# Kernel optimization log

Hardware: AMD Instinct MI355X
Metric: run time of the kernel (lower is better)

The kernel has to match this reference:

```python
import jax, jax.numpy as jnp
import numpy as np

# Standard SMPL kinematic tree (parent of joint i); root parent is -1.
PARENTS = [-1, 0, 0, 0, 1, 2, 3, 4, 5, 6, 7, 8, 9, 9, 9, 12, 13, 14, 16, 17, 18, 19, 20, 21]
NUM_JOINTS = 24
NUM_VERTICES = 6890
NUM_BETAS = 10
UNIT_FACTOR = 1.0  # unit='m'


def rotvec2mat(r):
    """Rodrigues formula. r: (..., 3) -> (..., 3, 3)."""
    theta = jnp.linalg.norm(r, axis=-1, keepdims=True)            # (..., 1)
    safe_theta = jnp.where(theta < 1e-8, 1.0, theta)
    axis = r / safe_theta
    x, y, z = axis[..., 0], axis[..., 1], axis[..., 2]
    zeros = jnp.zeros_like(x)
    K = jnp.stack([zeros, -z, y, z, zeros, -x, -y, x, zeros], axis=-1)
    K = K.reshape(r.shape[:-1] + (3, 3))
    t = theta[..., None]                                          # (..., 1, 1)
    eye = jnp.eye(3, dtype=r.dtype)
    return eye + jnp.sin(t) * K + (1.0 - jnp.cos(t)) * (K @ K)


def setup_inputs() -> dict:
    key = jax.random.key(0)
    ks = jax.random.split(key, 9)
    B = 1024
    pose_rotvecs = 0.3 * jax.random.normal(ks[0], (B, NUM_JOINTS, 3), jnp.float32)
    shape_betas = jax.random.normal(ks[1], (B, NUM_BETAS), jnp.float32)
    trans = jax.random.normal(ks[2], (B, 3), jnp.float32)
    v_template = jax.random.normal(ks[3], (NUM_VERTICES, 3), jnp.float32)
    shapedirs = 0.01 * jax.random.normal(ks[4], (NUM_VERTICES, 3, NUM_BETAS), jnp.float32)
    posedirs = 0.01 * jax.random.normal(ks[5], (NUM_VERTICES, 3, (NUM_JOINTS - 1) * 9), jnp.float32)
    J_template = jax.random.normal(ks[6], (NUM_JOINTS, 3), jnp.float32)
    J_shapedirs = 0.01 * jax.random.normal(ks[7], (NUM_JOINTS, 3, NUM_BETAS), jnp.float32)
    w = jax.random.uniform(ks[8], (NUM_VERTICES, NUM_JOINTS), jnp.float32)
    weights = w / jnp.sum(w, axis=-1, keepdims=True)  # skinning weights: rows sum to 1
    return dict(pose_rotvecs=pose_rotvecs, shape_betas=shape_betas, trans=trans,
                v_template=v_template, shapedirs=shapedirs, posedirs=posedirs,
                J_template=J_template, J_shapedirs=J_shapedirs, weights=weights)


def reference(pose_rotvecs, shape_betas, trans, v_template, shapedirs, posedirs,
              J_template, J_shapedirs, weights):
    B = pose_rotvecs.shape[0]
    parent_idx = jnp.asarray(PARENTS[1:], dtype=jnp.int32)  # (J-1,)

    # Parent-relative rotation matrices from rotation vectors.
    rel_rotmats = rotvec2mat(pose_rotvecs)                  # (B, J, 3, 3)

    # Kinematic chain: compose global rotations along the tree (J=24, fixed small loop).
    glob_list = [rel_rotmats[:, 0]]
    for i in range(1, NUM_JOINTS):
        glob_list.append(glob_list[PARENTS[i]] @ rel_rotmats[:, i])
    glob_rotmats = jnp.stack(glob_list, axis=1)             # (B, J, 3, 3)

    eye = jnp.broadcast_to(jnp.eye(3, dtype=rel_rotmats.dtype), (B, 1, 3, 3))
    parent_glob = jnp.concatenate([eye, glob_rotmats[:, parent_idx]], axis=1)  # (B, J, 3, 3)

    # Shaped joint locations (kid_factor = 0 default -> term vanishes).
    j = J_template + jnp.einsum('jcs,bs->bjc', J_shapedirs, shape_betas)       # (B, J, 3)
    j_parent = jnp.concatenate([jnp.zeros((B, 1, 3), j.dtype), j[:, parent_idx]], axis=1)
    bones = j - j_parent
    rotated_bones = jnp.einsum('bjCc,bjc->bjC', parent_glob, bones)

    pos_list = [j[:, 0]]
    for i in range(1, NUM_JOINTS):
        pos_list.append(pos_list[PARENTS[i]] + rotated_bones[:, i])
    glob_positions = jnp.stack(pos_list, axis=1)            # (B, J, 3)

    # Blendshapes: shape + pose correctives (kid term zero).
    pose_feature = rel_rotmats[:, 1:].reshape(B, (NUM_JOINTS - 1) * 9)
    v_posed = (v_template
               + jnp.einsum('vcp,bp->bvc', shapedirs, shape_betas)
               + jnp.einsum('vcp,bp->bvc', posedirs, pose_feature))            # (B, V, 3)

    # Linear blend skinning.
    translations = glob_positions - jnp.einsum('bjCc,bjc->bjC', glob_rotmats, j)  # (B, J, 3)
    blended_rot = jnp.einsum('vj,bjCc->bvCc', weights, glob_rotmats)              # (B, V, 3, 3)
    vertices = (jnp.einsum('bvCc,bvc->bvC', blended_rot, v_posed)
                + jnp.einsum('vj,bjc->bvc', weights, translations))               # (B, V, 3)

    joints = (glob_positions + trans[:, None]) * UNIT_FACTOR
    vertices = (vertices + trans[:, None]) * UNIT_FACTOR
    return joints, vertices, glob_rotmats
```

## Files before the change

### kernel.cpp

```cpp
#include <hip/hip_runtime.h>
#include <math.h>

#define NJ 24
#define NV 6890
#define NB 10
#define KREAL 217
#define KP 224
#define NVT 432

typedef __attribute__((ext_vector_type(8))) short bf16x8;
typedef __attribute__((ext_vector_type(8))) unsigned short u16x8;
typedef __attribute__((ext_vector_type(4))) float f32x4;

__device__ __forceinline__ unsigned short f2bf(float x) {
    unsigned int u = __float_as_uint(x);
    u += 0x7fffu + ((u >> 16) & 1u);
    return (unsigned short)(u >> 16);
}

__device__ __constant__ int c_path[NJ][9] = {
  {0,0,0,0,0,0,0,0,0},
  {0,1,0,0,0,0,0,0,0},
  {0,2,0,0,0,0,0,0,0},
  {0,3,0,0,0,0,0,0,0},
  {0,1,4,0,0,0,0,0,0},
  {0,2,5,0,0,0,0,0,0},
  {0,3,6,0,0,0,0,0,0},
  {0,1,4,7,0,0,0,0,0},
  {0,2,5,8,0,0,0,0,0},
  {0,3,6,9,0,0,0,0,0},
  {0,1,4,7,10,0,0,0,0},
  {0,2,5,8,11,0,0,0,0},
  {0,3,6,9,12,0,0,0,0},
  {0,3,6,9,13,0,0,0,0},
  {0,3,6,9,14,0,0,0,0},
  {0,3,6,9,12,15,0,0,0},
  {0,3,6,9,13,16,0,0,0},
  {0,3,6,9,14,17,0,0,0},
  {0,3,6,9,13,16,18,0,0},
  {0,3,6,9,14,17,19,0,0},
  {0,3,6,9,13,16,18,20,0},
  {0,3,6,9,14,17,19,21,0},
  {0,3,6,9,13,16,18,20,22},
  {0,3,6,9,14,17,19,21,23}};
__device__ __constant__ int c_plen[NJ] = {1,2,2,2,3,3,3,4,4,4,5,5,5,5,5,6,6,6,7,7,8,8,9,9};

__global__ __launch_bounds__(256)
void pack_kernel(const float* __restrict__ shapedirs, const float* __restrict__ posedirs,
                 unsigned short* __restrict__ dirsF)
{
    __shared__ unsigned short tile[16][3][240];
    const int t = threadIdx.x;
    const int vtg = blockIdx.x;

    for (int idx = t; idx < 16 * 3 * KP; idx += 256) {
        const int v_l = idx / (3 * KP);
        const int rem = idx - v_l * (3 * KP);
        const int c = rem / KP;
        const int k = rem - c * KP;
        const int v = vtg * 16 + v_l;
        float val = 0.f;
        if (v < NV && k < KREAL)
            val = (k < NB) ? shapedirs[(size_t)v * 30 + c * NB + k]
                           : posedirs[(size_t)v * 621 + c * 207 + (k - NB)];
        tile[v_l][c][k] = f2bf(val);
    }
    __syncthreads();

    const int lane = t & 63;
    const int w = t >> 6;
    const int kg = lane >> 4;
    const int vsub = lane & 15;
    for (int j2 = w; j2 < 21; j2 += 4) {
        const int kt = j2 / 3;
        const int c = j2 - kt * 3;
        const u16x8 o = *(const u16x8*)&tile[vsub][c][kt * 32 + kg * 8];
        *(u16x8*)&dirsF[(((size_t)(kt * 3 + c) * NVT + vtg) * 64 + lane) * 8] = o;
    }
}

__global__ __launch_bounds__(64)
void prep_kernel(const float* __restrict__ pose, const float* __restrict__ betas,
                 const float* __restrict__ trans, const float* __restrict__ J_template,
                 const float* __restrict__ J_shapedirs,
                 float* __restrict__ joints_out, float* __restrict__ glob_out,
                 float* __restrict__ A_ws, unsigned short* __restrict__ coeffF, int B)
{
    const int b = blockIdx.x;
    const int t = threadIdx.x;
    __shared__ float s_beta[NB];
    __shared__ float s_rel[NJ][9];
    __shared__ float s_glob[NJ][9];
    __shared__ float s_j[NJ][3];

    if (t < NB) s_beta[t] = betas[b * NB + t];
    __syncthreads();

    if (t < NJ) {
        float rx = pose[b * 72 + t * 3 + 0];
        float ry = pose[b * 72 + t * 3 + 1];
        float rz = pose[b * 72 + t * 3 + 2];
        float th = sqrtf(rx * rx + ry * ry + rz * rz);
        float safe = (th < 1e-8f) ? 1.0f : th;
        float ax = rx / safe, ay = ry / safe, az = rz / safe;
        float s = sinf(th), c = cosf(th), omc = 1.0f - c;
        float aa = ax * ax + ay * ay + az * az;
        float K[9] = {0.f, -az, ay, az, 0.f, -ax, -ay, ax, 0.f};
        float A2[9] = {ax*ax - aa, ax*ay,      ax*az,
                       ay*ax,      ay*ay - aa, ay*az,
                       az*ax,      az*ay,      az*az - aa};
        #pragma unroll
        for (int r = 0; r < 3; ++r)
            #pragma unroll
            for (int cc = 0; cc < 3; ++cc)
                s_rel[t][r * 3 + cc] = ((r == cc) ? 1.0f : 0.0f)
                                     + s * K[r * 3 + cc] + omc * A2[r * 3 + cc];
        #pragma unroll
        for (int cc = 0; cc < 3; ++cc) {
            float acc = J_template[t * 3 + cc];
            #pragma unroll
            for (int q = 0; q < NB; ++q)
                acc = fmaf(J_shapedirs[(t * 3 + cc) * NB + q], s_beta[q], acc);
            s_j[t][cc] = acc;
        }
    }
    __syncthreads();

    if (t < NJ) {
        const int L = c_plen[t];
        float G[9];
        #pragma unroll
        for (int e = 0; e < 9; ++e) G[e] = s_rel[0][e];
        for (int sIdx = 1; sIdx < L; ++sIdx) {
            const int p = c_path[t][sIdx];
            float Tn[9];
            #pragma unroll
            for (int r = 0; r < 3; ++r)
                #pragma unroll
                for (int cc = 0; cc < 3; ++cc)
                    Tn[r * 3 + cc] = G[r * 3 + 0] * s_rel[p][0 * 3 + cc]
                                   + G[r * 3 + 1] * s_rel[p][1 * 3 + cc]
                                   + G[r * 3 + 2] * s_rel[p][2 * 3 + cc];
            #pragma unroll
            for (int e = 0; e < 9; ++e) G[e] = Tn[e];
        }
        #pragma unroll
        for (int e = 0; e < 9; ++e) s_glob[t][e] = G[e];
        #pragma unroll
        for (int e = 0; e < 9; ++e) glob_out[(size_t)b * 216 + t * 9 + e] = G[e];
    }
    __syncthreads();

    if (t < NJ) {
        const int L = c_plen[t];
        float px = s_j[0][0], py = s_j[0][1], pz = s_j[0][2];
        for (int sIdx = 1; sIdx < L; ++sIdx) {
            const int pk = c_path[t][sIdx];
            const int pp = c_path[t][sIdx - 1];
            float bx = s_j[pk][0] - s_j[pp][0];
            float by = s_j[pk][1] - s_j[pp][1];
            float bz = s_j[pk][2] - s_j[pp][2];
            px += s_glob[pp][0] * bx + s_glob[pp][1] * by + s_glob[pp][2] * bz;
            py += s_glob[pp][3] * bx + s_glob[pp][4] * by + s_glob[pp][5] * bz;
            pz += s_glob[pp][6] * bx + s_glob[pp][7] * by + s_glob[pp][8] * bz;
        }
        const float tx = trans[b * 3 + 0], ty = trans[b * 3 + 1], tz = trans[b * 3 + 2];
        joints_out[(size_t)b * 72 + t * 3 + 0] = px + tx;
        joints_out[(size_t)b * 72 + t * 3 + 1] = py + ty;
        joints_out[(size_t)b * 72 + t * 3 + 2] = pz + tz;
        const float jx = s_j[t][0], jy = s_j[t][1], jz = s_j[t][2];
        float T0 = px - (s_glob[t][0] * jx + s_glob[t][1] * jy + s_glob[t][2] * jz) + tx;
        float T1 = py - (s_glob[t][3] * jx + s_glob[t][4] * jy + s_glob[t][5] * jz) + ty;
        float T2 = pz - (s_glob[t][6] * jx + s_glob[t][7] * jy + s_glob[t][8] * jz) + tz;
        float* Ab = A_ws + ((size_t)b * NJ + t) * 12;
        Ab[0]  = s_glob[t][0]; Ab[1]  = s_glob[t][1]; Ab[2]  = s_glob[t][2]; Ab[3]  = T0;
        Ab[4]  = s_glob[t][3]; Ab[5]  = s_glob[t][4]; Ab[6]  = s_glob[t][5]; Ab[7]  = T1;
        Ab[8]  = s_glob[t][6]; Ab[9]  = s_glob[t][7]; Ab[10] = s_glob[t][8]; Ab[11] = T2;
    }
    __syncthreads();

    const int btg = b >> 4, bl = b & 15;
    for (int k = t; k < KP; k += 64) {
        float val;
        if (k < NB) val = s_beta[k];
        else if (k < KREAL) { const int p2 = k - NB; val = s_rel[1 + p2 / 9][p2 % 9]; }
        else val = 0.f;
        const int kt = k >> 5, kg = (k >> 3) & 3, i = k & 7;
        coeffF[(((size_t)kt * (B >> 4) + btg) * 64 + kg * 16 + bl) * 8 + i] = f2bf(val);
    }
}

__global__ __launch_bounds__(256, 4)
void vert_kernel(const float4* __restrict__ dirsF, const float4* __restrict__ coeffF,
                 const float* __restrict__ A_ws, const float* __restrict__ v_template,
                 const float* __restrict__ weights, float* __restrict__ vert_out, int B)
{
    __shared__ float smem[6336];
    const int tid  = threadIdx.x;
    const int lane = tid & 63;
    const int w    = __builtin_amdgcn_readfirstlane(tid >> 6);
    const int vt   = w;
    const int vb4  = blockIdx.y * 4;
    const int bblk = blockIdx.x;
    const int nbt  = B >> 4;

    f32x4 acc[3][4];
    #pragma unroll
    for (int c = 0; c < 3; ++c)
        #pragma unroll
        for (int bt = 0; bt < 4; ++bt) {
            acc[c][bt][0] = 0.f; acc[c][bt][1] = 0.f; acc[c][bt][2] = 0.f; acc[c][bt][3] = 0.f;
        }

    for (int kt = 0; kt < 7; ++kt) {
        __syncthreads();
        #pragma unroll
        for (int s = 0; s < 3; ++s) {
            const int row = s * 256 + tid;
            const int ch = row >> 6, l2 = row & 63;
            *(float4*)&smem[row * 4] =
                dirsF[((size_t)(kt * 3 + (ch >> 2)) * NVT + vb4 + (ch & 3)) * 64 + l2];
        }
        __syncthreads();
        bf16x8 bq[4];
        #pragma unroll
        for (int bt = 0; bt < 4; ++bt)
            bq[bt] = *(const bf16x8*)&coeffF[((size_t)kt * nbt + bblk * 4 + bt) * 64 + lane];
        #pragma unroll
        for (int c = 0; c < 3; ++c) {
            const bf16x8 a = *(const bf16x8*)&smem[((c * 4 + vt) * 64 + lane) * 4];
            #pragma unroll
            for (int bt = 0; bt < 4; ++bt)
                acc[c][bt] = __builtin_amdgcn_mfma_f32_16x16x32_bf16(a, bq[bt], acc[c][bt], 0, 0, 0);
        }
    }

    const int vrow0 = (vb4 + vt) * 16 + ((lane >> 4) << 2);
    #pragma unroll
    for (int c = 0; c < 3; ++c) {
        float tv[4];
        #pragma unroll
        for (int r = 0; r < 4; ++r) {
            const int v = vrow0 + r;
            tv[r] = (v < NV) ? v_template[(size_t)v * 3 + c] : 0.f;
        }
        #pragma unroll
        for (int bt = 0; bt < 4; ++bt) {
            acc[c][bt][0] += tv[0]; acc[c][bt][1] += tv[1];
            acc[c][bt][2] += tv[2]; acc[c][bt][3] += tv[3];
        }
    }

    const int vglob = vb4 * 16 + lane;
    float wj[NJ];
    if (vglob < NV) {
        const float4* wp = (const float4*)(weights + (size_t)vglob * NJ);
        #pragma unroll
        for (int q = 0; q < 6; ++q) {
            const float4 t4 = wp[q];
            wj[q * 4 + 0] = t4.x; wj[q * 4 + 1] = t4.y; wj[q * 4 + 2] = t4.z; wj[q * 4 + 3] = t4.w;
        }
    }

    __syncthreads();

    for (int p = 0; p < 2; ++p) {
        if (p) __syncthreads();
        #pragma unroll
        for (int c = 0; c < 3; ++c)
            #pragma unroll
            for (int half = 0; half < 2; ++half) {
                const int b32 = half * 16 + (lane & 15);
                const int vl  = vt * 16 + ((lane >> 4) << 2);
                const f32x4 av = acc[c][2 * p + half];
                #pragma unroll
                for (int r = 0; r < 4; ++r)
                    smem[(c * 32 + b32) * 66 + vl + r] = av[r];
            }
        __syncthreads();

        if (vglob < NV) {
            for (int i = 0; i < 8; ++i) {
                const int b32 = w * 8 + i;
                const int b = bblk * 64 + p * 32 + b32;
                const float4* Ab = (const float4*)(A_ws + (size_t)b * (NJ * 12));
                float R0 = 0.f, R1 = 0.f, R2 = 0.f, R3 = 0.f, R4 = 0.f, R5 = 0.f,
                      R6 = 0.f, R7 = 0.f, R8 = 0.f, T0 = 0.f, T1 = 0.f, T2 = 0.f;
                #pragma unroll
                for (int jj = 0; jj < NJ; ++jj) {
                    const float wv = wj[jj];
                    const float4 a0 = Ab[jj * 3 + 0];
                    const float4 a1 = Ab[jj * 3 + 1];
                    const float4 a2 = Ab[jj * 3 + 2];
                    R0 = fmaf(wv, a0.x, R0); R1 = fmaf(wv, a0.y, R1); R2 = fmaf(wv, a0.z, R2); T0 = fmaf(wv, a0.w, T0);
                    R3 = fmaf(wv, a1.x, R3); R4 = fmaf(wv, a1.y, R4); R5 = fmaf(wv, a1.z, R5); T1 = fmaf(wv, a1.w, T1);
                    R6 = fmaf(wv, a2.x, R6); R7 = fmaf(wv, a2.y, R7); R8 = fmaf(wv, a2.z, R8); T2 = fmaf(wv, a2.w, T2);
                }
                const float vp0 = smem[(0 * 32 + b32) * 66 + lane];
                const float vp1 = smem[(1 * 32 + b32) * 66 + lane];
                const float vp2 = smem[(2 * 32 + b32) * 66 + lane];
                const float o0 = R0 * vp0 + R1 * vp1 + R2 * vp2 + T0;
                const float o1 = R3 * vp0 + R4 * vp1 + R5 * vp2 + T1;
                const float o2 = R6 * vp0 + R7 * vp1 + R8 * vp2 + T2;
                const size_t off = (size_t)b * (NV * 3) + (size_t)vglob * 3;
                vert_out[off + 0] = o0;
                vert_out[off + 1] = o1;
                vert_out[off + 2] = o2;
            }
        }
    }
}

extern "C" void kernel_launch(void* const* d_in, const int* in_sizes, int n_in,
                              void* d_out, int out_size, void* d_ws, size_t ws_size,
                              hipStream_t stream) {
    const float* pose        = (const float*)d_in[0];
    const float* betas       = (const float*)d_in[1];
    const float* trans       = (const float*)d_in[2];
    const float* v_template  = (const float*)d_in[3];
    const float* shapedirs   = (const float*)d_in[4];
    const float* posedirs    = (const float*)d_in[5];
    const float* J_template  = (const float*)d_in[6];
    const float* J_shapedirs = (const float*)d_in[7];
    const float* weights     = (const float*)d_in[8];
    const int B = in_sizes[0] / 72;

    float* out = (float*)d_out;
    float* joints_out = out;
    float* vert_out   = out + (size_t)B * 72;
    float* glob_out   = out + (size_t)B * 72 + (size_t)B * NV * 3;

    char* ws = (char*)d_ws;
    const size_t a_bytes     = (size_t)B * 288 * 4;
    const size_t coeff_bytes = (size_t)7 * (B >> 4) * 64 * 16;
    float*          A_ws   = (float*)ws;
    unsigned short* coeffF = (unsigned short*)(ws + a_bytes);
    unsigned short* dirsF  = (unsigned short*)(ws + a_bytes + coeff_bytes);

    pack_kernel<<<dim3(NVT), 256, 0, stream>>>(shapedirs, posedirs, dirsF);
    prep_kernel<<<dim3(B), 64, 0, stream>>>(pose, betas, trans, J_template, J_shapedirs,
                                            joints_out, glob_out, A_ws, coeffF, B);
    vert_kernel<<<dim3(B / 64, 108), 256, 0, stream>>>((const float4*)dirsF, (const float4*)coeffF,
                                                       A_ws, v_template, weights, vert_out, B);
}
```

Before: 221.4 us.

## Compute skinning blend with split-bf16 MFMA instead of scalar FMAs

```diff
diff --git a/kernel.cpp b/kernel.cpp
--- a/kernel.cpp
+++ b/kernel.cpp
@@ -16,6 +16,9 @@
     unsigned int u = __float_as_uint(x);
     u += 0x7fffu + ((u >> 16) & 1u);
     return (unsigned short)(u >> 16);
+}
+__device__ __forceinline__ float bf2f(unsigned short h) {
+    return __uint_as_float(((unsigned int)h) << 16);
 }
 
 __device__ __constant__ int c_path[NJ][9] = {
@@ -84,7 +87,8 @@
                  const float* __restrict__ trans, const float* __restrict__ J_template,
                  const float* __restrict__ J_shapedirs,
                  float* __restrict__ joints_out, float* __restrict__ glob_out,
-                 float* __restrict__ A_ws, unsigned short* __restrict__ coeffF, int B)
+                 unsigned short* __restrict__ AF, unsigned short* __restrict__ AFL,
+                 unsigned short* __restrict__ coeffF, int B)
 {
     const int b = blockIdx.x;
     const int t = threadIdx.x;
@@ -92,6 +96,7 @@
     __shared__ float s_rel[NJ][9];
     __shared__ float s_glob[NJ][9];
     __shared__ float s_j[NJ][3];
+    __shared__ float s_A[NJ][12];
 
     if (t < NB) s_beta[t] = betas[b * NB + t];
     __syncthreads();
@@ -172,14 +177,13 @@
         float T0 = px - (s_glob[t][0] * jx + s_glob[t][1] * jy + s_glob[t][2] * jz) + tx;
         float T1 = py - (s_glob[t][3] * jx + s_glob[t][4] * jy + s_glob[t][5] * jz) + ty;
         float T2 = pz - (s_glob[t][6] * jx + s_glob[t][7] * jy + s_glob[t][8] * jz) + tz;
-        float* Ab = A_ws + ((size_t)b * NJ + t) * 12;
-        Ab[0]  = s_glob[t][0]; Ab[1]  = s_glob[t][1]; Ab[2]  = s_glob[t][2]; Ab[3]  = T0;
-        Ab[4]  = s_glob[t][3]; Ab[5]  = s_glob[t][4]; Ab[6]  = s_glob[t][5]; Ab[7]  = T1;
-        Ab[8]  = s_glob[t][6]; Ab[9]  = s_glob[t][7]; Ab[10] = s_glob[t][8]; Ab[11] = T2;
-    }
-    __syncthreads();
-
-    const int btg = b >> 4, bl = b & 15;
+        s_A[t][0]  = s_glob[t][0]; s_A[t][1]  = s_glob[t][1]; s_A[t][2]  = s_glob[t][2]; s_A[t][3]  = T0;
+        s_A[t][4]  = s_glob[t][3]; s_A[t][5]  = s_glob[t][4]; s_A[t][6]  = s_glob[t][5]; s_A[t][7]  = T1;
+        s_A[t][8]  = s_glob[t][6]; s_A[t][9]  = s_glob[t][7]; s_A[t][10] = s_glob[t][8]; s_A[t][11] = T2;
+    }
+    __syncthreads();
+
+    const int btg = b >> 4, bl = b & 15, bt_ = (b >> 4) & 3;
     for (int k = t; k < KP; k += 64) {
         float val;
         if (k < NB) val = s_beta[k];
@@ -188,12 +192,25 @@
         const int kt = k >> 5, kg = (k >> 3) & 3, i = k & 7;
         coeffF[(((size_t)kt * (B >> 4) + btg) * 64 + kg * 16 + bl) * 8 + i] = f2bf(val);
     }
-}
-
-__global__ __launch_bounds__(256, 4)
+    for (int idx = t; idx < 12 * 32; idx += 64) {
+        const int e = idx >> 5, jj = idx & 31, kg = jj >> 3, i = jj & 7;
+        const float val = (jj < NJ) ? s_A[jj][e] : 0.f;
+        AF[((((size_t)(b >> 6) * 12 + e) * 4 + bt_) * 64 + kg * 16 + bl) * 8 + i] = f2bf(val);
+    }
+    for (int idx = t; idx < 3 * 32; idx += 64) {
+        const int et = idx >> 5, jj = idx & 31, kg = jj >> 3, i = jj & 7;
+        const float val = (jj < NJ) ? s_A[jj][et * 4 + 3] : 0.f;
+        const unsigned short hi = f2bf(val);
+        AFL[((((size_t)(b >> 6) * 3 + et) * 4 + bt_) * 64 + kg * 16 + bl) * 8 + i]
+            = f2bf(val - bf2f(hi));
+    }
+}
+
+__global__ __launch_bounds__(256)
 void vert_kernel(const float4* __restrict__ dirsF, const float4* __restrict__ coeffF,
-                 const float* __restrict__ A_ws, const float* __restrict__ v_template,
-                 const float* __restrict__ weights, float* __restrict__ vert_out, int B)
+                 const float4* __restrict__ AF, const float4* __restrict__ AFL,
+                 const float* __restrict__ v_template, const float* __restrict__ weights,
+                 float* __restrict__ vert_out, int B)
 {
     __shared__ float smem[6336];
     const int tid  = threadIdx.x;
@@ -251,57 +268,73 @@
         }
     }
 
+    bf16x8 wh, wl;
+    {
+        const int vA = (vb4 + vt) * 16 + (lane & 15);
+        const int kg = lane >> 4;
+        if (kg < 3 && vA < NV) {
+            const float* wp = weights + (size_t)vA * NJ + kg * 8;
+            #pragma unroll
+            for (int i = 0; i < 8; ++i) {
+                const float val = wp[i];
+                const unsigned short hi = f2bf(val);
+                wh[i] = (short)hi;
+                wl[i] = (short)f2bf(val - bf2f(hi));
+            }
+        } else {
+            #pragma unroll
+            for (int i = 0; i < 8; ++i) { wh[i] = 0; wl[i] = 0; }
+        }
+    }
+
+    __syncthreads();
+
+    f32x4 zero; zero[0] = 0.f; zero[1] = 0.f; zero[2] = 0.f; zero[3] = 0.f;
     const int vglob = vb4 * 16 + lane;
-    float wj[NJ];
-    if (vglob < NV) {
-        const float4* wp = (const float4*)(weights + (size_t)vglob * NJ);
-        #pragma unroll
-        for (int q = 0; q < 6; ++q) {
-            const float4 t4 = wp[q];
-            wj[q * 4 + 0] = t4.x; wj[q * 4 + 1] = t4.y; wj[q * 4 + 2] = t4.z; wj[q * 4 + 3] = t4.w;
-        }
-    }
-
-    __syncthreads();
 
     for (int p = 0; p < 2; ++p) {
         if (p) __syncthreads();
         #pragma unroll
-        for (int c = 0; c < 3; ++c)
-            #pragma unroll
-            for (int half = 0; half < 2; ++half) {
+        for (int half = 0; half < 2; ++half) {
+            const int bt = 2 * p + half;
+            #pragma unroll
+            for (int C = 0; C < 3; ++C) {
+                const size_t baseT  = (((size_t)bblk * 12 + (C * 4 + 3)) * 4 + bt) * 64 + lane;
+                const size_t baseTL = (((size_t)bblk * 3 + C) * 4 + bt) * 64 + lane;
+                const bf16x8 ATh = *(const bf16x8*)&AF[baseT];
+                const bf16x8 ATl = *(const bf16x8*)&AFL[baseTL];
+                f32x4 out = __builtin_amdgcn_mfma_f32_16x16x32_bf16(wl, ATh, zero, 0, 0, 0);
+                out = __builtin_amdgcn_mfma_f32_16x16x32_bf16(wh, ATl, out, 0, 0, 0);
+                out = __builtin_amdgcn_mfma_f32_16x16x32_bf16(wh, ATh, out, 0, 0, 0);
+                #pragma unroll
+                for (int q = 0; q < 3; ++q) {
+                    const size_t baseR = (((size_t)bblk * 12 + (C * 4 + q)) * 4 + bt) * 64 + lane;
+                    const bf16x8 ARh = *(const bf16x8*)&AF[baseR];
+                    f32x4 rr = __builtin_amdgcn_mfma_f32_16x16x32_bf16(wl, ARh, zero, 0, 0, 0);
+                    rr = __builtin_amdgcn_mfma_f32_16x16x32_bf16(wh, ARh, rr, 0, 0, 0);
+                    out[0] = fmaf(rr[0], acc[q][bt][0], out[0]);
+                    out[1] = fmaf(rr[1], acc[q][bt][1], out[1]);
+                    out[2] = fmaf(rr[2], acc[q][bt][2], out[2]);
+                    out[3] = fmaf(rr[3], acc[q][bt][3], out[3]);
+                }
                 const int b32 = half * 16 + (lane & 15);
                 const int vl  = vt * 16 + ((lane >> 4) << 2);
-                const f32x4 av = acc[c][2 * p + half];
-                #pragma unroll
-                for (int r = 0; r < 4; ++r)
-                    smem[(c * 32 + b32) * 66 + vl + r] = av[r];
+                smem[(C * 32 + b32) * 66 + vl + 0] = out[0];
+                smem[(C * 32 + b32) * 66 + vl + 1] = out[1];
+                smem[(C * 32 + b32) * 66 + vl + 2] = out[2];
+                smem[(C * 32 + b32) * 66 + vl + 3] = out[3];
             }
+        }
         __syncthreads();
 
         if (vglob < NV) {
+            #pragma unroll
             for (int i = 0; i < 8; ++i) {
                 const int b32 = w * 8 + i;
                 const int b = bblk * 64 + p * 32 + b32;
-                const float4* Ab = (const float4*)(A_ws + (size_t)b * (NJ * 12));
-                float R0 = 0.f, R1 = 0.f, R2 = 0.f, R3 = 0.f, R4 = 0.f, R5 = 0.f,
-                      R6 = 0.f, R7 = 0.f, R8 = 0.f, T0 = 0.f, T1 = 0.f, T2 = 0.f;
-                #pragma unroll
-                for (int jj = 0; jj < NJ; ++jj) {
-                    const float wv = wj[jj];
-                    const float4 a0 = Ab[jj * 3 + 0];
-                    const float4 a1 = Ab[jj * 3 + 1];
-                    const float4 a2 = Ab[jj * 3 + 2];
-                    R0 = fmaf(wv, a0.x, R0); R1 = fmaf(wv, a0.y, R1); R2 = fmaf(wv, a0.z, R2); T0 = fmaf(wv, a0.w, T0);
-                    R3 = fmaf(wv, a1.x, R3); R4 = fmaf(wv, a1.y, R4); R5 = fmaf(wv, a1.z, R5); T1 = fmaf(wv, a1.w, T1);
-                    R6 = fmaf(wv, a2.x, R6); R7 = fmaf(wv, a2.y, R7); R8 = fmaf(wv, a2.z, R8); T2 = fmaf(wv, a2.w, T2);
-                }
-                const float vp0 = smem[(0 * 32 + b32) * 66 + lane];
-                const float vp1 = smem[(1 * 32 + b32) * 66 + lane];
-                const float vp2 = smem[(2 * 32 + b32) * 66 + lane];
-                const float o0 = R0 * vp0 + R1 * vp1 + R2 * vp2 + T0;
-                const float o1 = R3 * vp0 + R4 * vp1 + R5 * vp2 + T1;
-                const float o2 = R6 * vp0 + R7 * vp1 + R8 * vp2 + T2;
+                const float o0 = smem[(0 * 32 + b32) * 66 + lane];
+                const float o1 = smem[(1 * 32 + b32) * 66 + lane];
+                const float o2 = smem[(2 * 32 + b32) * 66 + lane];
                 const size_t off = (size_t)b * (NV * 3) + (size_t)vglob * 3;
                 vert_out[off + 0] = o0;
                 vert_out[off + 1] = o1;
@@ -331,15 +364,18 @@
     float* glob_out   = out + (size_t)B * 72 + (size_t)B * NV * 3;
 
     char* ws = (char*)d_ws;
-    const size_t a_bytes     = (size_t)B * 288 * 4;
     const size_t coeff_bytes = (size_t)7 * (B >> 4) * 64 * 16;
-    float*          A_ws   = (float*)ws;
-    unsigned short* coeffF = (unsigned short*)(ws + a_bytes);
-    unsigned short* dirsF  = (unsigned short*)(ws + a_bytes + coeff_bytes);
+    const size_t af_bytes    = (size_t)(B >> 6) * 12 * 4 * 64 * 16;
+    const size_t afl_bytes   = (size_t)(B >> 6) * 3 * 4 * 64 * 16;
+    unsigned short* coeffF = (unsigned short*)ws;
+    unsigned short* AF     = (unsigned short*)(ws + coeff_bytes);
+    unsigned short* AFL    = (unsigned short*)(ws + coeff_bytes + af_bytes);
+    unsigned short* dirsF  = (unsigned short*)(ws + coeff_bytes + af_bytes + afl_bytes);
 
     pack_kernel<<<dim3(NVT), 256, 0, stream>>>(shapedirs, posedirs, dirsF);
     prep_kernel<<<dim3(B), 64, 0, stream>>>(pose, betas, trans, J_template, J_shapedirs,
-                                            joints_out, glob_out, A_ws, coeffF, B);
+                                            joints_out, glob_out, AF, AFL, coeffF, B);
     vert_kernel<<<dim3(B / 64, 108), 256, 0, stream>>>((const float4*)dirsF, (const float4*)coeffF,
-                                                       A_ws, v_template, weights, vert_out, B);
-}
+                                                       (const float4*)AF, (const float4*)AFL,
+                                                       v_template, weights, vert_out, B);
+}
```

New measurement: 223.0 us. No clear change (+0.7%).
